# Optimization experiments

Measured on AMD Instinct MI355X. Metric: run time of the kernel, lower is better.

## Reference

```python
import jax, jax.numpy as jnp
import numpy as np

B, S, D_IN, D_OUT = 4, 2048, 1024, 1024

def setup_inputs() -> dict:
    key = jax.random.key(0)
    k1, k2, k3, k4 = jax.random.split(key, 4)
    sc = 0.02
    return {
        "x": jax.random.normal(k1, (B, S, D_IN), dtype=jnp.float32),
        "Wq": jax.random.normal(k2, (D_OUT, D_IN), dtype=jnp.float32) * sc,
        "Wk": jax.random.normal(k3, (D_OUT, D_IN), dtype=jnp.float32) * sc,
        "Wv": jax.random.normal(k4, (D_OUT, D_IN), dtype=jnp.float32) * sc,
    }

def reference(x, Wq, Wk, Wv):
    # torch Linear: y = x @ W.T  (weights stored [out, in])
    b, n, _ = x.shape
    q = jnp.einsum('bnd,od->bno', x, Wq)  # [B,S,D_OUT]
    k = jnp.einsum('bnd,od->bno', x, Wk)
    v = jnp.einsum('bnd,od->bno', x, Wv)
    scores = jnp.einsum('bqd,bkd->bqk', q, k)  # [B,S,S]
    # causal mask: positions j > i masked to -inf BEFORE scaling (matches source)
    causal = jnp.triu(jnp.ones((n, n), dtype=bool), k=1)
    scores = jnp.where(causal[None, :, :], -jnp.inf, scores)
    scale = 1.0 / jnp.sqrt(jnp.float32(k.shape[-1]))
    attn = jax.nn.softmax(scores * scale, axis=-1)
    # NOTE: source calls dropout but discards its output -> no-op
    return jnp.einsum('bqk,bkd->bqd', attn, v)
```

## Files before the change

kernel.cpp:

```cpp
#include <hip/hip_runtime.h>
#include <hip/hip_bf16.h>
#include <hip/hip_fp16.h>


using bf16 = __hip_bfloat16;
typedef __bf16 bf16x8 __attribute__((ext_vector_type(8)));
typedef float f32x4 __attribute__((ext_vector_type(4)));

__device__ __forceinline__ void load_lds_16B(const void* g, void* l) {
  __builtin_amdgcn_global_load_lds(
      (const __attribute__((address_space(1))) unsigned int*)g,
      (__attribute__((address_space(3))) unsigned int*)l, 16, 0, 0);
}

template <int N>
__device__ __forceinline__ void waitcnt_vm() {
  if constexpr (N == 8) asm volatile("s_waitcnt vmcnt(8)" ::: "memory");
  else if constexpr (N == 6) asm volatile("s_waitcnt vmcnt(6)" ::: "memory");
  else if constexpr (N == 5) asm volatile("s_waitcnt vmcnt(5)" ::: "memory");
  else asm volatile("s_waitcnt vmcnt(0)" ::: "memory");
}

__device__ __forceinline__ int swz(int o) { return o ^ (((o >> 7) & 7) << 4); }

template <int BM, int BN, int WM, int WN, int STHR, int OCC, int OUT,
          bool CSKIP, bool KLIM, int NPASS>
__global__ __launch_bounds__(WM* WN * 64, OCC) void gemmT(
    const bf16* __restrict__ A, const bf16* __restrict__ Bm, void* __restrict__ Cv,
    int K, int lda, int ldb, int ldc, long sAz, long sBz, long sCzBytes) {
  constexpr int MR = BM / WM / 16, NR = BN / WN / 16, MH2 = MR / 2;
  constexpr int AKC = BM * 64;
  constexpr int BKC = BN * 64;
  constexpr int DBSTR = 2 * (AKC + BKC);
  constexpr int CHUNK = STHR * 16;
  constexpr int ACALLS = AKC / CHUNK;
  constexpr int BCALLS = BKC / CHUNK;
  constexpr int VM_LEAVE = ACALLS + 2 * BCALLS;

  const int tn = blockIdx.x, z = blockIdx.z;
  if (CSKIP && (long)tn * BN >= (long)blockIdx.y * BM + BM) return;
  A += (long)z * sAz;
  Bm += (long)z * sBz;
  char* C = (char*)Cv + (long)z * sCzBytes;

  __shared__ __align__(128) char sm[2 * DBSTR];
  const int tid = threadIdx.x, lane = tid & 63, wv = tid >> 6;
  const int wr = wv / WN, wc = wv % WN;
  const int ldsw = wv * 1024;
  const int ts = (tid < STHR) ? tid : 0;

  int aoff[MR], boff[NR];
#pragma unroll
  for (int m = 0; m < MR; m++)
    aoff[m] = swz((wr * (BM / WM) + m * 16 + (lane & 15)) * 64 + (lane >> 4) * 16);
#pragma unroll
  for (int n = 0; n < NR; n++)
    boff[n] = 2 * AKC + swz((wc * (BN / WN) + n * 16 + (lane & 15)) * 64 + (lane >> 4) * 16);

  const char* srcB[BCALLS];
#pragma unroll
  for (int c = 0; c < BCALLS; c++) {
    int os = swz(c * CHUNK + ts * 16);
    srcB[c] = (const char*)(Bm + ((long)tn * BN + (os >> 6)) * ldb) + (os & 63);
  }

  for (int pass = 0; pass < NPASS; ++pass) {
    const int tm = (NPASS == 2)
                       ? (pass == 0 ? blockIdx.y : 2 * (int)gridDim.y - 1 - (int)blockIdx.y)
                       : (int)blockIdx.y;

    int kEnd = K;
    if (KLIM) kEnd = min(tm * BM + BM, K);
    int nt = kEnd >> 6;
    if (KLIM) nt = (nt + 1) & ~1;
    const int NI = nt >> 1;

    const char* srcA[ACALLS];
#pragma unroll
    for (int c = 0; c < ACALLS; c++) {
      int os = swz(c * CHUNK + ts * 16);
      srcA[c] = (const char*)(A + ((long)tm * BM + (os >> 6)) * lda) + (os & 63);
    }
    auto stageA = [&](int t, int kc) {
      if (tid < STHR) {
#pragma unroll
        for (int c = 0; c < ACALLS; c++)
          load_lds_16B(srcA[c] + (long)t * 128 + kc * 64,
                       sm + (t & 1) * DBSTR + kc * AKC + c * CHUNK + ldsw);
      }
    };
    auto stageB = [&](int t, int kc) {
      if (tid < STHR) {
#pragma unroll
        for (int c = 0; c < BCALLS; c++)
          load_lds_16B(srcB[c] + (long)t * 128 + kc * 64,
                       sm + (t & 1) * DBSTR + 2 * AKC + kc * BKC + c * CHUNK + ldsw);
      }
    };

    f32x4 acc[MR][NR] = {};
    bf16x8 bfr[2][NR];
    bf16x8 afrA[MH2], afrB[MH2];

#define LDB(DBUF, KC)                                                          \
  _Pragma("unroll") for (int n = 0; n < NR; n++)                               \
      bfr[KC][n] = *(const bf16x8*)(sm + (DBUF)*DBSTR + (KC)*BKC + boff[n]);
#define LDA(DBUF, KC, MH, DST)                                                 \
  _Pragma("unroll") for (int m = 0; m < MH2; m++)                              \
      DST[m] = *(const bf16x8*)(sm + (DBUF)*DBSTR + (KC)*AKC + aoff[(MH)*MH2 + m]);
#define MFMAS(KC, MH, AFR)                                                     \
  __builtin_amdgcn_s_setprio(1);                                               \
  _Pragma("unroll") for (int m = 0; m < MH2; m++)                              \
      _Pragma("unroll") for (int n = 0; n < NR; n++)                           \
          acc[(MH)*MH2 + m][n] = __builtin_amdgcn_mfma_f32_16x16x32_bf16(      \
              AFR[m], bfr[KC][n], acc[(MH)*MH2 + m][n], 0, 0, 0);              \
  __builtin_amdgcn_s_setprio(0);
#define BAR1()                                                                 \
  __builtin_amdgcn_s_barrier();                                                \
  asm volatile("s_waitcnt lgkmcnt(0)" ::: "memory");                           \
  __builtin_amdgcn_sched_barrier(0);
#define BAR2() __builtin_amdgcn_s_barrier();

    stageB(0, 0); stageA(0, 0); stageB(0, 1); stageA(0, 1);
    stageB(1, 0); stageA(1, 0); stageB(1, 1);
    waitcnt_vm<VM_LEAVE>();
    __builtin_amdgcn_s_barrier();

    for (int i = 0; i < NI - 1; i++) {
      const int ta = 2 * i, tb = 2 * i + 1;
      LDB(0, 0); LDA(0, 0, 0, afrA); stageA(tb, 1);     BAR1(); MFMAS(0, 0, afrA); BAR2();
      LDA(0, 0, 1, afrB);            stageB(ta + 2, 0); BAR1(); MFMAS(0, 1, afrB); BAR2();
      LDB(0, 1); LDA(0, 1, 0, afrA); stageA(ta + 2, 0); BAR1(); MFMAS(1, 0, afrA); BAR2();
      LDA(0, 1, 1, afrB);            stageB(ta + 2, 1);
      waitcnt_vm<VM_LEAVE>();                           BAR1(); MFMAS(1, 1, afrB); BAR2();
      LDB(1, 0); LDA(1, 0, 0, afrA); stageA(ta + 2, 1); BAR1(); MFMAS(0, 0, afrA); BAR2();
      LDA(1, 0, 1, afrB);            stageB(tb + 2, 0); BAR1(); MFMAS(0, 1, afrB); BAR2();
      LDB(1, 1); LDA(1, 1, 0, afrA); stageA(tb + 2, 0); BAR1(); MFMAS(1, 0, afrA); BAR2();
      LDA(1, 1, 1, afrB);            stageB(tb + 2, 1);
      waitcnt_vm<VM_LEAVE>();                           BAR1(); MFMAS(1, 1, afrB); BAR2();
    }
    {
      const int tb = nt - 1;
      LDB(0, 0); LDA(0, 0, 0, afrA); stageA(tb, 1); BAR1(); MFMAS(0, 0, afrA); BAR2();
      LDA(0, 0, 1, afrB);                           BAR1(); MFMAS(0, 1, afrB); BAR2();
      LDB(0, 1); LDA(0, 1, 0, afrA);                BAR1(); MFMAS(1, 0, afrA); BAR2();
      LDA(0, 1, 1, afrB); waitcnt_vm<0>();          BAR1(); MFMAS(1, 1, afrB); BAR2();
      LDB(1, 0); LDA(1, 0, 0, afrA);                BAR1(); MFMAS(0, 0, afrA); BAR2();
      LDA(1, 0, 1, afrB);                           BAR1(); MFMAS(0, 1, afrB); BAR2();
      LDB(1, 1); LDA(1, 1, 0, afrA);                BAR1(); MFMAS(1, 0, afrA); BAR2();
      LDA(1, 1, 1, afrB);                           BAR1(); MFMAS(1, 1, afrB); BAR2();
    }
#undef LDB
#undef LDA
#undef MFMAS
#undef BAR1
#undef BAR2

    const int cr0 = tm * BM + wr * (BM / WM) + (lane >> 4) * 4;
    const int cc0 = tn * BN + wc * (BN / WN) + (lane & 15);
#pragma unroll
    for (int m = 0; m < MR; m++)
#pragma unroll
      for (int n = 0; n < NR; n++)
#pragma unroll
        for (int j = 0; j < 4; j++) {
          long row = cr0 + m * 16 + j;
          long col = cc0 + n * 16;
          if (OUT == 1)
            ((bf16*)C)[row * (long)ldc + col] = __float2bfloat16(acc[m][n][j]);
          else if (OUT == 2)
            ((__half*)C)[row * (long)ldc + col] = __float2half(acc[m][n][j]);
          else
            ((float*)C)[row * (long)ldc + col] = acc[m][n][j];
        }
  }
}

__global__ __launch_bounds__(256) void cvt_all(const float* __restrict__ x,
                                               const float* __restrict__ wq,
                                               const float* __restrict__ wk,
                                               const float* __restrict__ wv,
                                               bf16* __restrict__ xb,
                                               bf16* __restrict__ wb) {
  const int b = blockIdx.x;
  const float* src;
  bf16* dst;
  int i;
  if (b < 8192) { src = x; dst = xb; i = b * 256 + threadIdx.x; }
  else if (b < 9216) { src = wq; dst = wb; i = (b - 8192) * 256 + threadIdx.x; }
  else if (b < 10240) { src = wk; dst = wb + 1048576; i = (b - 9216) * 256 + threadIdx.x; }
  else { src = wv; dst = wb + 2097152; i = (b - 10240) * 256 + threadIdx.x; }
  float4 f = ((const float4*)src)[i];
  union { bf16 h[4]; uint2 u; } o;
  o.h[0] = __float2bfloat16(f.x);
  o.h[1] = __float2bfloat16(f.y);
  o.h[2] = __float2bfloat16(f.z);
  o.h[3] = __float2bfloat16(f.w);
  ((uint2*)dst)[i] = o.u;
}

typedef short short4v __attribute__((ext_vector_type(4)));

__global__ __launch_bounds__(256) void softmax_causal(const __half* __restrict__ Sc,
                                                      bf16* __restrict__ P) {
  const int i = blockIdx.x, b = blockIdx.y;
  const long base = ((long)b * 2048 + i) * 2048;
  const __half* row = Sc + base;
  bf16* prow = P + base;
  const int tid = threadIdx.x, lane = tid & 63, wv = tid >> 6;
  const int len = i + 1;

  float v[8];
  float m = -3.3e38f;
  {
    const int j0 = tid * 8;
    union { short4v s[2]; __half h[8]; } u;
    u.s[0] = *(const short4v*)(row + j0);
    u.s[1] = *(const short4v*)(row + j0 + 4);
#pragma unroll
    for (int e = 0; e < 8; e++) {
      float t = __half2float(u.h[e]);
      v[e] = (j0 + e < len) ? t : -3.3e38f;
      m = fmaxf(m, v[e]);
    }
  }
  for (int o = 32; o; o >>= 1) m = fmaxf(m, __shfl_xor(m, o));
  __shared__ float redm[4], reds[4];
  if (lane == 0) redm[wv] = m;
  __syncthreads();
  m = fmaxf(fmaxf(redm[0], redm[1]), fmaxf(redm[2], redm[3]));

  const float scale = 0.03125f;
  float e8[8];
  float s = 0.f;
  {
    const int j0 = tid * 8;
#pragma unroll
    for (int e = 0; e < 8; e++) {
      float t = (j0 + e < len) ? __expf((v[e] - m) * scale) : 0.f;
      e8[e] = t;
      s += t;
    }
  }
  for (int o = 32; o; o >>= 1) s += __shfl_xor(s, o);
  if (lane == 0) reds[wv] = s;
  __syncthreads();
  s = reds[0] + reds[1] + reds[2] + reds[3];
  const float inv = 1.0f / s;
  {
    const int j0 = tid * 8;
    union { bf16 h[8]; uint4 u4; } o;
#pragma unroll
    for (int e = 0; e < 8; e++) o.h[e] = __float2bfloat16(e8[e] * inv);
    *(uint4*)(prow + j0) = o.u4;
  }
}

__global__ __launch_bounds__(256) void transposeV(const bf16* __restrict__ V,
                                                  bf16* __restrict__ Vt) {
  __shared__ bf16 t[32][33];
  const int b = blockIdx.z;
  const int s0 = blockIdx.x << 5;
  const int d0 = blockIdx.y << 5;
  const bf16* Vb = V + (long)b * 2048 * 3072;
  bf16* Vtb = Vt + (long)b * 1024 * 2048;
  const int lx = threadIdx.x & 31, ly = threadIdx.x >> 5;
#pragma unroll
  for (int r = 0; r < 32; r += 8)
    t[r + ly][lx] = Vb[(long)(s0 + r + ly) * 3072 + d0 + lx];
  __syncthreads();
#pragma unroll
  for (int r = 0; r < 32; r += 8)
    Vtb[(long)(d0 + r + ly) * 2048 + s0 + lx] = t[lx][r + ly];
}

extern "C" void kernel_launch(void* const* d_in, const int* in_sizes, int n_in,
                              void* d_out, int out_size, void* d_ws, size_t ws_size,
                              hipStream_t stream) {
  const float* x = (const float*)d_in[0];
  const float* Wq = (const float*)d_in[1];
  const float* Wk = (const float*)d_in[2];
  const float* Wv = (const float*)d_in[3];

  const long MBy = 1 << 20;
  char* ws = (char*)d_ws;
  bf16* Cqkv = (bf16*)(ws);
  bf16* Vt = (bf16*)(ws + 48 * MBy);
  bf16* P = (bf16*)(ws + 64 * MBy);
  __half* Sc = (__half*)(ws + 96 * MBy);
  bf16* xb = (bf16*)(ws + 96 * MBy);
  bf16* Wb = (bf16*)(ws + 112 * MBy);

  cvt_all<<<11264, 256, 0, stream>>>(x, Wq, Wk, Wv, xb, Wb);

  gemmT<128, 128, 2, 2, 256, 2, 1, false, false, 1><<<dim3(24, 64), 256, 0, stream>>>(
      xb, Wb, Cqkv, 1024, 1024, 1024, 3072, 0L, 0L, 0L);

  transposeV<<<dim3(64, 32, 4), 256, 0, stream>>>(Cqkv + 2048, Vt);

  gemmT<128, 128, 2, 2, 256, 2, 2, true, false, 1><<<dim3(16, 16, 4), 256, 0, stream>>>(
      Cqkv, Cqkv + 1024, Sc, 1024, 3072, 3072, 2048,
      2048L * 3072, 2048L * 3072, 2048L * 2048 * 2);

  softmax_causal<<<dim3(2048, 4), 256, 0, stream>>>(Sc, P);

  gemmT<128, 128, 2, 2, 256, 2, 0, false, true, 2><<<dim3(8, 8, 4), 256, 0, stream>>>(
      P, Vt, d_out, 2048, 2048, 2048, 1024,
      2048L * 2048, 1024L * 2048, 2048L * 1024 * 4);
}
```

Before: 163.3 us.

## Pipeline multiple output tiles per block without draining between tiles

Adds a persistent-style GEMM kernel that walks several output tiles in one continuous K-loop, prefetching the next tile's operands while finishing the current one, and writes each tile's accumulator when its K range ends. The QKV projection now uses 128x256 tiles with 512 threads and three N-tiles per block. The PV GEMM pairs a short and a long causal row tile without restarting the pipeline between them. This targets the prologue/epilogue bubbles and tail imbalance of per-tile launches, at the cost of more registers, LDS and index bookkeeping, plus fewer, larger blocks in the QKV GEMM.

```diff
diff --git a/kernel.cpp b/kernel.cpp
--- a/kernel.cpp
+++ b/kernel.cpp
@@ -15,92 +15,12 @@
 
 template <int N>
 __device__ __forceinline__ void waitcnt_vm() {
-  if constexpr (N == 8) asm volatile("s_waitcnt vmcnt(8)" ::: "memory");
-  else if constexpr (N == 6) asm volatile("s_waitcnt vmcnt(6)" ::: "memory");
+  if constexpr (N == 6) asm volatile("s_waitcnt vmcnt(6)" ::: "memory");
   else if constexpr (N == 5) asm volatile("s_waitcnt vmcnt(5)" ::: "memory");
   else asm volatile("s_waitcnt vmcnt(0)" ::: "memory");
 }
 
 __device__ __forceinline__ int swz(int o) { return o ^ (((o >> 7) & 7) << 4); }
-
-template <int BM, int BN, int WM, int WN, int STHR, int OCC, int OUT,
-          bool CSKIP, bool KLIM, int NPASS>
-__global__ __launch_bounds__(WM* WN * 64, OCC) void gemmT(
-    const bf16* __restrict__ A, const bf16* __restrict__ Bm, void* __restrict__ Cv,
-    int K, int lda, int ldb, int ldc, long sAz, long sBz, long sCzBytes) {
-  constexpr int MR = BM / WM / 16, NR = BN / WN / 16, MH2 = MR / 2;
-  constexpr int AKC = BM * 64;
-  constexpr int BKC = BN * 64;
-  constexpr int DBSTR = 2 * (AKC + BKC);
-  constexpr int CHUNK = STHR * 16;
-  constexpr int ACALLS = AKC / CHUNK;
-  constexpr int BCALLS = BKC / CHUNK;
-  constexpr int VM_LEAVE = ACALLS + 2 * BCALLS;
-
-  const int tn = blockIdx.x, z = blockIdx.z;
-  if (CSKIP && (long)tn * BN >= (long)blockIdx.y * BM + BM) return;
-  A += (long)z * sAz;
-  Bm += (long)z * sBz;
-  char* C = (char*)Cv + (long)z * sCzBytes;
-
-  __shared__ __align__(128) char sm[2 * DBSTR];
-  const int tid = threadIdx.x, lane = tid & 63, wv = tid >> 6;
-  const int wr = wv / WN, wc = wv % WN;
-  const int ldsw = wv * 1024;
-  const int ts = (tid < STHR) ? tid : 0;
-
-  int aoff[MR], boff[NR];
-#pragma unroll
-  for (int m = 0; m < MR; m++)
-    aoff[m] = swz((wr * (BM / WM) + m * 16 + (lane & 15)) * 64 + (lane >> 4) * 16);
-#pragma unroll
-  for (int n = 0; n < NR; n++)
-    boff[n] = 2 * AKC + swz((wc * (BN / WN) + n * 16 + (lane & 15)) * 64 + (lane >> 4) * 16);
-
-  const char* srcB[BCALLS];
-#pragma unroll
-  for (int c = 0; c < BCALLS; c++) {
-    int os = swz(c * CHUNK + ts * 16);
-    srcB[c] = (const char*)(Bm + ((long)tn * BN + (os >> 6)) * ldb) + (os & 63);
-  }
-
-  for (int pass = 0; pass < NPASS; ++pass) {
-    const int tm = (NPASS == 2)
-                       ? (pass == 0 ? blockIdx.y : 2 * (int)gridDim.y - 1 - (int)blockIdx.y)
-                       : (int)blockIdx.y;
-
-    int kEnd = K;
-    if (KLIM) kEnd = min(tm * BM + BM, K);
-    int nt = kEnd >> 6;
-    if (KLIM) nt = (nt + 1) & ~1;
-    const int NI = nt >> 1;
-
-    const char* srcA[ACALLS];
-#pragma unroll
-    for (int c = 0; c < ACALLS; c++) {
-      int os = swz(c * CHUNK + ts * 16);
-      srcA[c] = (const char*)(A + ((long)tm * BM + (os >> 6)) * lda) + (os & 63);
-    }
-    auto stageA = [&](int t, int kc) {
-      if (tid < STHR) {
-#pragma unroll
-        for (int c = 0; c < ACALLS; c++)
-          load_lds_16B(srcA[c] + (long)t * 128 + kc * 64,
-                       sm + (t & 1) * DBSTR + kc * AKC + c * CHUNK + ldsw);
-      }
-    };
-    auto stageB = [&](int t, int kc) {
-      if (tid < STHR) {
-#pragma unroll
-        for (int c = 0; c < BCALLS; c++)
-          load_lds_16B(srcB[c] + (long)t * 128 + kc * 64,
-                       sm + (t & 1) * DBSTR + 2 * AKC + kc * BKC + c * CHUNK + ldsw);
-      }
-    };
-
-    f32x4 acc[MR][NR] = {};
-    bf16x8 bfr[2][NR];
-    bf16x8 afrA[MH2], afrB[MH2];
 
 #define LDB(DBUF, KC)                                                          \
   _Pragma("unroll") for (int n = 0; n < NR; n++)                               \
@@ -121,59 +41,278 @@
   __builtin_amdgcn_sched_barrier(0);
 #define BAR2() __builtin_amdgcn_s_barrier();
 
-    stageB(0, 0); stageA(0, 0); stageB(0, 1); stageA(0, 1);
-    stageB(1, 0); stageA(1, 0); stageB(1, 1);
-    waitcnt_vm<VM_LEAVE>();
-    __builtin_amdgcn_s_barrier();
-
-    for (int i = 0; i < NI - 1; i++) {
-      const int ta = 2 * i, tb = 2 * i + 1;
-      LDB(0, 0); LDA(0, 0, 0, afrA); stageA(tb, 1);     BAR1(); MFMAS(0, 0, afrA); BAR2();
-      LDA(0, 0, 1, afrB);            stageB(ta + 2, 0); BAR1(); MFMAS(0, 1, afrB); BAR2();
-      LDB(0, 1); LDA(0, 1, 0, afrA); stageA(ta + 2, 0); BAR1(); MFMAS(1, 0, afrA); BAR2();
-      LDA(0, 1, 1, afrB);            stageB(ta + 2, 1);
-      waitcnt_vm<VM_LEAVE>();                           BAR1(); MFMAS(1, 1, afrB); BAR2();
-      LDB(1, 0); LDA(1, 0, 0, afrA); stageA(ta + 2, 1); BAR1(); MFMAS(0, 0, afrA); BAR2();
-      LDA(1, 0, 1, afrB);            stageB(tb + 2, 0); BAR1(); MFMAS(0, 1, afrB); BAR2();
-      LDB(1, 1); LDA(1, 1, 0, afrA); stageA(tb + 2, 0); BAR1(); MFMAS(1, 0, afrA); BAR2();
-      LDA(1, 1, 1, afrB);            stageB(tb + 2, 1);
-      waitcnt_vm<VM_LEAVE>();                           BAR1(); MFMAS(1, 1, afrB); BAR2();
-    }
-    {
-      const int tb = nt - 1;
-      LDB(0, 0); LDA(0, 0, 0, afrA); stageA(tb, 1); BAR1(); MFMAS(0, 0, afrA); BAR2();
-      LDA(0, 0, 1, afrB);                           BAR1(); MFMAS(0, 1, afrB); BAR2();
-      LDB(0, 1); LDA(0, 1, 0, afrA);                BAR1(); MFMAS(1, 0, afrA); BAR2();
-      LDA(0, 1, 1, afrB); waitcnt_vm<0>();          BAR1(); MFMAS(1, 1, afrB); BAR2();
-      LDB(1, 0); LDA(1, 0, 0, afrA);                BAR1(); MFMAS(0, 0, afrA); BAR2();
-      LDA(1, 0, 1, afrB);                           BAR1(); MFMAS(0, 1, afrB); BAR2();
-      LDB(1, 1); LDA(1, 1, 0, afrA);                BAR1(); MFMAS(1, 0, afrA); BAR2();
-      LDA(1, 1, 1, afrB);                           BAR1(); MFMAS(1, 1, afrB); BAR2();
-    }
-#undef LDB
-#undef LDA
-#undef MFMAS
-#undef BAR1
-#undef BAR2
-
-    const int cr0 = tm * BM + wr * (BM / WM) + (lane >> 4) * 4;
-    const int cc0 = tn * BN + wc * (BN / WN) + (lane & 15);
+template <int BM, int BN, int WM, int WN, int STHR, int OCC, int OUT, int MODE>
+__global__ __launch_bounds__(WM* WN * 64, OCC) void gemmP(
+    const bf16* __restrict__ A, const bf16* __restrict__ Bm, void* __restrict__ Cv,
+    int K, int lda, int ldb, int ldc, long sAz, long sBz, long sCzBytes) {
+  constexpr int TILES = (MODE == 0) ? 3 : 2;
+  constexpr int MR = BM / WM / 16, NR = BN / WN / 16, MH2 = MR / 2;
+  constexpr int AKC = BM * 64;
+  constexpr int BKC = BN * 64;
+  constexpr int DBSTR = 2 * (AKC + BKC);
+  constexpr int CHUNK = STHR * 16;
+  constexpr int ACALLS = AKC / CHUNK;
+  constexpr int BCALLS = BKC / CHUNK;
+  constexpr int VM_LEAVE = ACALLS + 2 * BCALLS;
+
+  const int bx = blockIdx.x, by = blockIdx.y, z = blockIdx.z;
+  A += (long)z * sAz;
+  Bm += (long)z * sBz;
+  char* C = (char*)Cv + (long)z * sCzBytes;
+
+  int tmA[TILES], tnA[TILES], ntA[TILES];
+#pragma unroll
+  for (int j = 0; j < TILES; j++) {
+    if (MODE == 0) {
+      tmA[j] = by;
+      tnA[j] = 3 * bx + j;
+      ntA[j] = K >> 6;
+    } else {
+      tmA[j] = (j == 0) ? by : (2 * (int)gridDim.y - 1 - by);
+      tnA[j] = bx;
+      ntA[j] = 2 * (tmA[j] + 1);
+    }
+  }
+  int S_total = 0;
+#pragma unroll
+  for (int j = 0; j < TILES; j++) S_total += ntA[j];
+  const int NI_tot = S_total >> 1;
+
+  __shared__ __align__(128) char sm[2 * DBSTR];
+  const int tid = threadIdx.x, lane = tid & 63, wv = tid >> 6;
+  const int wr = wv / WN, wc = wv % WN;
+  const int ldsw = wv * 1024;
+  const int ts = (tid < STHR) ? tid : 0;
+
+  const char* baseA[ACALLS];
+  const char* baseB[BCALLS];
+#pragma unroll
+  for (int c = 0; c < ACALLS; c++) {
+    int os = swz(c * CHUNK + ts * 16);
+    baseA[c] = (const char*)(A + (long)(os >> 6) * lda) + (os & 63);
+  }
+#pragma unroll
+  for (int c = 0; c < BCALLS; c++) {
+    int os = swz(c * CHUNK + ts * 16);
+    baseB[c] = (const char*)(Bm + (long)(os >> 6) * ldb) + (os & 63);
+  }
+  long AJ[TILES], BJ[TILES];
+#pragma unroll
+  for (int j = 0; j < TILES; j++) {
+    AJ[j] = (long)tmA[j] * BM * lda * 2;
+    BJ[j] = (long)tnA[j] * BN * ldb * 2;
+  }
+
+  auto mapg = [&](int g, int& j, int& t) {
+    if (MODE == 0) { j = g >> 4; t = g & 15; }
+    else { j = (g >= ntA[0]) ? 1 : 0; t = g - (j ? ntA[0] : 0); }
+  };
+  auto stA = [&](int g, int kc) {
+    if (tid < STHR) {
+      int j, t; mapg(g, j, t);
+#pragma unroll
+      for (int c = 0; c < ACALLS; c++)
+        load_lds_16B(baseA[c] + AJ[j] + (long)t * 128 + kc * 64,
+                     sm + (g & 1) * DBSTR + kc * AKC + c * CHUNK + ldsw);
+    }
+  };
+  auto stB = [&](int g, int kc) {
+    if (tid < STHR) {
+      int j, t; mapg(g, j, t);
+#pragma unroll
+      for (int c = 0; c < BCALLS; c++)
+        load_lds_16B(baseB[c] + BJ[j] + (long)t * 128 + kc * 64,
+                     sm + (g & 1) * DBSTR + 2 * AKC + kc * BKC + c * CHUNK + ldsw);
+    }
+  };
+
+  int aoff[MR], boff[NR];
+#pragma unroll
+  for (int m = 0; m < MR; m++)
+    aoff[m] = swz((wr * (BM / WM) + m * 16 + (lane & 15)) * 64 + (lane >> 4) * 16);
+#pragma unroll
+  for (int n = 0; n < NR; n++)
+    boff[n] = 2 * AKC + swz((wc * (BN / WN) + n * 16 + (lane & 15)) * 64 + (lane >> 4) * 16);
+
+  f32x4 acc[MR][NR] = {};
+  bf16x8 bfr[2][NR];
+  bf16x8 afrA[MH2], afrB[MH2];
+
+  auto writeC = [&](int j) {
+    const int cr0 = tmA[j] * BM + wr * (BM / WM) + (lane >> 4) * 4;
+    const int cc0 = tnA[j] * BN + wc * (BN / WN) + (lane & 15);
 #pragma unroll
     for (int m = 0; m < MR; m++)
 #pragma unroll
-      for (int n = 0; n < NR; n++)
-#pragma unroll
-        for (int j = 0; j < 4; j++) {
-          long row = cr0 + m * 16 + j;
+      for (int n = 0; n < NR; n++) {
+#pragma unroll
+        for (int jj = 0; jj < 4; jj++) {
+          long row = cr0 + m * 16 + jj;
           long col = cc0 + n * 16;
           if (OUT == 1)
-            ((bf16*)C)[row * (long)ldc + col] = __float2bfloat16(acc[m][n][j]);
-          else if (OUT == 2)
-            ((__half*)C)[row * (long)ldc + col] = __float2half(acc[m][n][j]);
+            ((bf16*)C)[row * (long)ldc + col] = __float2bfloat16(acc[m][n][jj]);
           else
-            ((float*)C)[row * (long)ldc + col] = acc[m][n][j];
+            ((float*)C)[row * (long)ldc + col] = acc[m][n][jj];
         }
-  }
+        acc[m][n] = f32x4{0.f, 0.f, 0.f, 0.f};
+      }
+  };
+
+  stB(0, 0); stA(0, 0); stB(0, 1); stA(0, 1);
+  stB(1, 0); stA(1, 0); stB(1, 1);
+  waitcnt_vm<VM_LEAVE>();
+  __builtin_amdgcn_s_barrier();
+
+  int curJ = 0, nextB = ntA[0];
+  for (int i = 0; i < NI_tot - 1; i++) {
+    const int ta = 2 * i, tb = 2 * i + 1;
+    LDB(0, 0); LDA(0, 0, 0, afrA); stA(tb, 1);     BAR1(); MFMAS(0, 0, afrA); BAR2();
+    LDA(0, 0, 1, afrB);            stB(ta + 2, 0); BAR1(); MFMAS(0, 1, afrB); BAR2();
+    LDB(0, 1); LDA(0, 1, 0, afrA); stA(ta + 2, 0); BAR1(); MFMAS(1, 0, afrA); BAR2();
+    LDA(0, 1, 1, afrB);            stB(ta + 2, 1);
+    waitcnt_vm<VM_LEAVE>();                        BAR1(); MFMAS(1, 1, afrB); BAR2();
+    LDB(1, 0); LDA(1, 0, 0, afrA); stA(ta + 2, 1); BAR1(); MFMAS(0, 0, afrA); BAR2();
+    LDA(1, 0, 1, afrB);            stB(tb + 2, 0); BAR1(); MFMAS(0, 1, afrB); BAR2();
+    LDB(1, 1); LDA(1, 1, 0, afrA); stB(tb + 2, 1); BAR1(); MFMAS(1, 0, afrA); BAR2();
+    LDA(1, 1, 1, afrB);            stA(tb + 2, 0);
+    waitcnt_vm<VM_LEAVE>();                        BAR1(); MFMAS(1, 1, afrB); BAR2();
+    if (tb + 1 == nextB) {
+      writeC(curJ);
+      curJ++;
+      if (curJ < TILES) nextB += ntA[curJ];
+    }
+  }
+  {
+    const int tb = S_total - 1;
+    LDB(0, 0); LDA(0, 0, 0, afrA); stA(tb, 1); BAR1(); MFMAS(0, 0, afrA); BAR2();
+    LDA(0, 0, 1, afrB);                        BAR1(); MFMAS(0, 1, afrB); BAR2();
+    LDB(0, 1); LDA(0, 1, 0, afrA);             BAR1(); MFMAS(1, 0, afrA); BAR2();
+    LDA(0, 1, 1, afrB); waitcnt_vm<0>();       BAR1(); MFMAS(1, 1, afrB); BAR2();
+    LDB(1, 0); LDA(1, 0, 0, afrA);             BAR1(); MFMAS(0, 0, afrA); BAR2();
+    LDA(1, 0, 1, afrB);                        BAR1(); MFMAS(0, 1, afrB); BAR2();
+    LDB(1, 1); LDA(1, 1, 0, afrA);             BAR1(); MFMAS(1, 0, afrA); BAR2();
+    LDA(1, 1, 1, afrB);                        BAR1(); MFMAS(1, 1, afrB); BAR2();
+  }
+  writeC(curJ);
+}
+
+template <int BM, int BN, int WM, int WN, int STHR, int OCC, int OUT,
+          bool CSKIP>
+__global__ __launch_bounds__(WM* WN * 64, OCC) void gemmT(
+    const bf16* __restrict__ A, const bf16* __restrict__ Bm, void* __restrict__ Cv,
+    int K, int lda, int ldb, int ldc, long sAz, long sBz, long sCzBytes) {
+  constexpr int MR = BM / WM / 16, NR = BN / WN / 16, MH2 = MR / 2;
+  constexpr int AKC = BM * 64;
+  constexpr int BKC = BN * 64;
+  constexpr int DBSTR = 2 * (AKC + BKC);
+  constexpr int CHUNK = STHR * 16;
+  constexpr int ACALLS = AKC / CHUNK;
+  constexpr int BCALLS = BKC / CHUNK;
+  constexpr int VM_LEAVE = ACALLS + 2 * BCALLS;
+
+  const int tn = blockIdx.x, tm = blockIdx.y, z = blockIdx.z;
+  if (CSKIP && (long)tn * BN >= (long)tm * BM + BM) return;
+  A += (long)z * sAz;
+  Bm += (long)z * sBz;
+  char* C = (char*)Cv + (long)z * sCzBytes;
+
+  const int nt = K >> 6;
+  const int NI = nt >> 1;
+
+  __shared__ __align__(128) char sm[2 * DBSTR];
+  const int tid = threadIdx.x, lane = tid & 63, wv = tid >> 6;
+  const int wr = wv / WN, wc = wv % WN;
+  const int ldsw = wv * 1024;
+  const int ts = (tid < STHR) ? tid : 0;
+
+  const char* srcA[ACALLS];
+  const char* srcB[BCALLS];
+#pragma unroll
+  for (int c = 0; c < ACALLS; c++) {
+    int os = swz(c * CHUNK + ts * 16);
+    srcA[c] = (const char*)(A + ((long)tm * BM + (os >> 6)) * lda) + (os & 63);
+  }
+#pragma unroll
+  for (int c = 0; c < BCALLS; c++) {
+    int os = swz(c * CHUNK + ts * 16);
+    srcB[c] = (const char*)(Bm + ((long)tn * BN + (os >> 6)) * ldb) + (os & 63);
+  }
+  auto stA = [&](int t, int kc) {
+    if (tid < STHR) {
+#pragma unroll
+      for (int c = 0; c < ACALLS; c++)
+        load_lds_16B(srcA[c] + (long)t * 128 + kc * 64,
+                     sm + (t & 1) * DBSTR + kc * AKC + c * CHUNK + ldsw);
+    }
+  };
+  auto stB = [&](int t, int kc) {
+    if (tid < STHR) {
+#pragma unroll
+      for (int c = 0; c < BCALLS; c++)
+        load_lds_16B(srcB[c] + (long)t * 128 + kc * 64,
+                     sm + (t & 1) * DBSTR + 2 * AKC + kc * BKC + c * CHUNK + ldsw);
+    }
+  };
+
+  int aoff[MR], boff[NR];
+#pragma unroll
+  for (int m = 0; m < MR; m++)
+    aoff[m] = swz((wr * (BM / WM) + m * 16 + (lane & 15)) * 64 + (lane >> 4) * 16);
+#pragma unroll
+  for (int n = 0; n < NR; n++)
+    boff[n] = 2 * AKC + swz((wc * (BN / WN) + n * 16 + (lane & 15)) * 64 + (lane >> 4) * 16);
+
+  f32x4 acc[MR][NR] = {};
+  bf16x8 bfr[2][NR];
+  bf16x8 afrA[MH2], afrB[MH2];
+
+  stB(0, 0); stA(0, 0); stB(0, 1); stA(0, 1);
+  stB(1, 0); stA(1, 0); stB(1, 1);
+  waitcnt_vm<VM_LEAVE>();
+  __builtin_amdgcn_s_barrier();
+
+  for (int i = 0; i < NI - 1; i++) {
+    const int ta = 2 * i, tb = 2 * i + 1;
+    LDB(0, 0); LDA(0, 0, 0, afrA); stA(tb, 1);     BAR1(); MFMAS(0, 0, afrA); BAR2();
+    LDA(0, 0, 1, afrB);            stB(ta + 2, 0); BAR1(); MFMAS(0, 1, afrB); BAR2();
+    LDB(0, 1); LDA(0, 1, 0, afrA); stA(ta + 2, 0); BAR1(); MFMAS(1, 0, afrA); BAR2();
+    LDA(0, 1, 1, afrB);            stB(ta + 2, 1);
+    waitcnt_vm<VM_LEAVE>();                        BAR1(); MFMAS(1, 1, afrB); BAR2();
+    LDB(1, 0); LDA(1, 0, 0, afrA); stA(ta + 2, 1); BAR1(); MFMAS(0, 0, afrA); BAR2();
+    LDA(1, 0, 1, afrB);            stB(tb + 2, 0); BAR1(); MFMAS(0, 1, afrB); BAR2();
+    LDB(1, 1); LDA(1, 1, 0, afrA); stB(tb + 2, 1); BAR1(); MFMAS(1, 0, afrA); BAR2();
+    LDA(1, 1, 1, afrB);            stA(tb + 2, 0);
+    waitcnt_vm<VM_LEAVE>();                        BAR1(); MFMAS(1, 1, afrB); BAR2();
+  }
+  {
+    const int tb = nt - 1;
+    LDB(0, 0); LDA(0, 0, 0, afrA); stA(tb, 1); BAR1(); MFMAS(0, 0, afrA); BAR2();
+    LDA(0, 0, 1, afrB);                        BAR1(); MFMAS(0, 1, afrB); BAR2();
+    LDB(0, 1); LDA(0, 1, 0, afrA);             BAR1(); MFMAS(1, 0, afrA); BAR2();
+    LDA(0, 1, 1, afrB); waitcnt_vm<0>();       BAR1(); MFMAS(1, 1, afrB); BAR2();
+    LDB(1, 0); LDA(1, 0, 0, afrA);             BAR1(); MFMAS(0, 0, afrA); BAR2();
+    LDA(1, 0, 1, afrB);                        BAR1(); MFMAS(0, 1, afrB); BAR2();
+    LDB(1, 1); LDA(1, 1, 0, afrA);             BAR1(); MFMAS(1, 0, afrA); BAR2();
+    LDA(1, 1, 1, afrB);                        BAR1(); MFMAS(1, 1, afrB); BAR2();
+  }
+
+  const int cr0 = tm * BM + wr * (BM / WM) + (lane >> 4) * 4;
+  const int cc0 = tn * BN + wc * (BN / WN) + (lane & 15);
+#pragma unroll
+  for (int m = 0; m < MR; m++)
+#pragma unroll
+    for (int n = 0; n < NR; n++)
+#pragma unroll
+      for (int j = 0; j < 4; j++) {
+        long row = cr0 + m * 16 + j;
+        long col = cc0 + n * 16;
+        if (OUT == 1)
+          ((bf16*)C)[row * (long)ldc + col] = __float2bfloat16(acc[m][n][j]);
+        else if (OUT == 2)
+          ((__half*)C)[row * (long)ldc + col] = __float2half(acc[m][n][j]);
+        else
+          ((float*)C)[row * (long)ldc + col] = acc[m][n][j];
+      }
 }
 
 __global__ __launch_bounds__(256) void cvt_all(const float* __restrict__ x,
@@ -293,18 +432,18 @@
 
   cvt_all<<<11264, 256, 0, stream>>>(x, Wq, Wk, Wv, xb, Wb);
 
-  gemmT<128, 128, 2, 2, 256, 2, 1, false, false, 1><<<dim3(24, 64), 256, 0, stream>>>(
+  gemmP<128, 256, 2, 4, 512, 2, 1, 0><<<dim3(4, 64), 512, 0, stream>>>(
       xb, Wb, Cqkv, 1024, 1024, 1024, 3072, 0L, 0L, 0L);
 
   transposeV<<<dim3(64, 32, 4), 256, 0, stream>>>(Cqkv + 2048, Vt);
 
-  gemmT<128, 128, 2, 2, 256, 2, 2, true, false, 1><<<dim3(16, 16, 4), 256, 0, stream>>>(
+  gemmT<128, 128, 2, 2, 256, 2, 2, true><<<dim3(16, 16, 4), 256, 0, stream>>>(
       Cqkv, Cqkv + 1024, Sc, 1024, 3072, 3072, 2048,
       2048L * 3072, 2048L * 3072, 2048L * 2048 * 2);
 
   softmax_causal<<<dim3(2048, 4), 256, 0, stream>>>(Sc, P);
 
-  gemmT<128, 128, 2, 2, 256, 2, 0, false, true, 2><<<dim3(8, 8, 4), 256, 0, stream>>>(
+  gemmP<128, 128, 2, 2, 256, 2, 0, 1><<<dim3(8, 8, 4), 256, 0, stream>>>(
       P, Vt, d_out, 2048, 2048, 2048, 1024,
       2048L * 2048, 1024L * 2048, 2048L * 1024 * 4);
 }
```

Result: no change. 165.5 us (+1.4%).
